# Kernel optimization log

Hardware: AMD Instinct MI355X
Metric: run time of the kernel (lower is better)

Reference implementation:

```python
import jax, jax.numpy as jnp
import numpy as np

B, L = 4, 2048
D_Q = D_K = D_V = 512
D_MODEL = 512
H = 8  # heads; head dim = D_MODEL // H = 64


def _conv1x1(x, W, b):
    # Conv1d with kernel_size=1 == pointwise linear over channels.
    # x: (B, C_in, L), W: (C_out, C_in), b: (C_out,) -> (B, C_out, L)
    return jnp.einsum('oc,bcl->bol', W, x) + b[None, :, None]


def setup_inputs() -> dict:
    key = jax.random.key(0)
    ks = jax.random.split(key, 12)
    s = 0.02
    return {
        'q': jax.random.normal(ks[0], (B, D_Q, L), jnp.float32),
        'k': jax.random.normal(ks[1], (B, D_K, L), jnp.float32),
        'v': jax.random.normal(ks[2], (B, D_V, L), jnp.float32),
        'input_mask': jnp.ones((B, 1, L), jnp.float32),
        'Wq': jax.random.normal(ks[3], (D_MODEL, D_Q), jnp.float32) * s,
        'bq': jax.random.normal(ks[4], (D_MODEL,), jnp.float32) * s,
        'Wk': jax.random.normal(ks[5], (D_MODEL, D_K), jnp.float32) * s,
        'bk': jax.random.normal(ks[6], (D_MODEL,), jnp.float32) * s,
        'Wv': jax.random.normal(ks[7], (D_MODEL, D_V), jnp.float32) * s,
        'bv': jax.random.normal(ks[8], (D_MODEL,), jnp.float32) * s,
        'Wout': jax.random.normal(ks[9], (D_V, D_MODEL), jnp.float32) * s,
        'bout': jax.random.normal(ks[10], (D_V,), jnp.float32) * s,
    }


def reference(q, k, v, input_mask, Wq, bq, Wk, bk, Wv, bv, Wout, bout):
    Bq, _, Lq = q.shape
    qh = _conv1x1(q, Wq, bq).reshape(Bq, H, -1, Lq)  # (B,H,D,L)
    kh = _conv1x1(k, Wk, bk).reshape(Bq, H, -1, Lq)
    vh = _conv1x1(v, Wv, bv).reshape(Bq, H, -1, Lq)
    Dh = qh.shape[2]
    scale = 1.0 / jnp.sqrt(jnp.asarray(Dh, qh.dtype))
    scores = jnp.einsum('bhdl,bhdn->bhln', qh, kh) * scale  # (B,H,L,L)
    # total_mask = ~input_mask[:, 0:1, :].bool(); True -> masked keys
    pad = input_mask[:, 0:1, :] <= 0.5  # (B,1,L_k)
    scores = jnp.where(pad[:, None, :, :], jnp.asarray(-1e9, scores.dtype), scores)
    attn = jax.nn.softmax(scores, axis=-1)  # attn_dropout is None in module
    out = jnp.einsum('bhdn,bhln->bhdl', vh, attn).reshape(Bq, -1, Lq)  # (B,d_model,L)
    # self.dropout is identity at inference; final 1x1 conv projection
    return _conv1x1(out, Wout, bout)  # (B, d_v, L)
```

## Files before the change

kernel.cpp:

```cpp
#include <hip/hip_runtime.h>
#include <hip/hip_bf16.h>


#define BB  4
#define LL  2048
#define CC  512
#define HH  8
#define DHH 64

typedef __attribute__((ext_vector_type(8)))  short bf16x8;
typedef __attribute__((ext_vector_type(4)))  short bf16x4;
typedef __attribute__((ext_vector_type(16))) float f32x16;
typedef __attribute__((ext_vector_type(2)))  unsigned uint2v;
typedef __attribute__((ext_vector_type(4)))  unsigned uint4v;

using us = unsigned short;

#if __has_builtin(__builtin_amdgcn_exp2f)
#define EXP2(x) __builtin_amdgcn_exp2f(x)
#else
#define EXP2(x) __expf(0.6931471805599453f * (x))
#endif

__device__ __forceinline__ us f2bu(float x) {
    unsigned u = __float_as_uint(x);
    return (us)((u + 0x7FFFu + ((u >> 16) & 1u)) >> 16);
}
__device__ __forceinline__ unsigned pk2(float a, float b) {
    unsigned r;
    asm("v_cvt_pk_bf16_f32 %0, %1, %2" : "=v"(r) : "v"(a), "v"(b));
    return r;
}
__device__ __forceinline__ bf16x4 pk4(float a, float b, float c, float d) {
    uint2v u; u[0] = pk2(a, b); u[1] = pk2(c, d);
    return __builtin_bit_cast(bf16x4, u);
}

__device__ __forceinline__ void gl16(const void* g, void* l) {
    __builtin_amdgcn_global_load_lds(
        (const __attribute__((address_space(1))) unsigned int*)g,
        (__attribute__((address_space(3))) unsigned int*)l, 16, 0, 0);
}

__device__ __forceinline__ void transpose_body(const float* __restrict__ X,
                                               us* __restrict__ Xt,
                                               int b, int c0, int n0, int t)
{
    __shared__ float T[64][65];

    const float* Xb = X + ((size_t)b * CC + c0) * LL + n0;
    #pragma unroll
    for (int i = 0; i < 4; ++i) {
        const int cl = (t >> 4) + 16 * i, nl = (t & 15) * 4;
        const float4 f = *(const float4*)(Xb + (size_t)cl * LL + nl);
        T[cl][nl + 0] = f.x; T[cl][nl + 1] = f.y;
        T[cl][nl + 2] = f.z; T[cl][nl + 3] = f.w;
    }
    __syncthreads();
    us* Ot = Xt + ((size_t)b * LL + n0) * CC + c0;
    #pragma unroll
    for (int i = 0; i < 2; ++i) {
        const int nl = (t >> 3) + 32 * i, cb = (t & 7) * 8;
        uint4v u;
        #pragma unroll
        for (int j = 0; j < 4; ++j)
            u[j] = pk2(T[cb + 2 * j][nl], T[cb + 2 * j + 1][nl]);
        *(bf16x8*)(Ot + (size_t)nl * CC + cb) = __builtin_bit_cast(bf16x8, u);
    }
}

__global__ __launch_bounds__(256) void transpose_cvt(const float* __restrict__ X,
                                                     us* __restrict__ Xt)
{
    transpose_body(X, Xt, blockIdx.z, blockIdx.y * 64, blockIdx.x * 64, threadIdx.x);
}

__global__ __launch_bounds__(256) void transpose_cvt3(
    const float* __restrict__ Xq, const float* __restrict__ Xk,
    const float* __restrict__ Xv,
    us* __restrict__ X0, us* __restrict__ X1, us* __restrict__ X2)
{
    const int z = blockIdx.z, which = z >> 2, b = z & 3;
    const float* X = which == 0 ? Xq : (which == 1 ? Xk : Xv);
    us* Xt = which == 0 ? X0 : (which == 1 ? X1 : X2);
    transpose_body(X, Xt, b, blockIdx.y * 64, blockIdx.x * 64, threadIdx.x);
}

__global__ __launch_bounds__(256) void cvt_w4(const float* __restrict__ W0,
                                              const float* __restrict__ W1,
                                              const float* __restrict__ W2,
                                              const float* __restrict__ W3,
                                              us* __restrict__ out)
{
    const float* Ws[4] = {W0, W1, W2, W3};
    const float* W = Ws[blockIdx.y];
    us* O = out + (size_t)blockIdx.y * (CC * CC);
    const int i = (blockIdx.x * 256 + threadIdx.x) * 8;
    const float4 f0 = *(const float4*)(W + i);
    const float4 f1 = *(const float4*)(W + i + 4);
    uint4v u;
    u[0] = pk2(f0.x, f0.y); u[1] = pk2(f0.z, f0.w);
    u[2] = pk2(f1.x, f1.y); u[3] = pk2(f1.z, f1.w);
    *(bf16x8*)(O + i) = __builtin_bit_cast(bf16x8, u);
}

__device__ __forceinline__ void proj_body(const us* __restrict__ Xb,
                                          const us* __restrict__ Wm,
                                          const float* __restrict__ bias,
                                          float scale, void* __restrict__ Yv,
                                          int b, int n0, int m0, int t, int mode)
{
    const int lane = t & 63, wave = t >> 6;
    const int quad2 = lane >> 5, l31 = lane & 31;
    const int wr = (wave >> 1) * 64, wc = (wave & 1) * 64;

    __shared__ __align__(16) char PS[32768];
    __shared__ float biasS[128];

    f32x16 acc[2][2];
    #pragma unroll
    for (int mi = 0; mi < 2; ++mi)
        #pragma unroll
        for (int ni = 0; ni < 2; ++ni)
            #pragma unroll
            for (int e = 0; e < 16; ++e) acc[mi][ni][e] = 0.f;

    if (t < 128) biasS[t] = bias[m0 + t];

    const int rdA = quad2 * 2048 + (wr + l31) * 16;
    const int rdB = 16384 + quad2 * 2048 + (wc + l31) * 16;

    for (int k0 = 0; k0 < CC; k0 += 64) {
        #pragma unroll
        for (int i = 0; i < 4; ++i) {
            const int sg = i * 4 + wave;
            const int r0 = (sg & 1) * 64, bk = sg >> 1;
            gl16(Wm + (size_t)(r0 + lane) * CC + k0 + bk * 8, PS + sg * 1024);
            gl16(Xb + (size_t)(n0 + r0 + lane) * CC + k0 + bk * 8,
                 PS + 16384 + sg * 1024);
        }
        __syncthreads();

        __builtin_amdgcn_s_setprio(1);
        #pragma unroll
        for (int ks = 0; ks < 4; ++ks) {
            const bf16x8 af0 = *(const bf16x8*)(PS + rdA + ks * 4096);
            const bf16x8 af1 = *(const bf16x8*)(PS + rdA + ks * 4096 + 512);
            const bf16x8 bf0 = *(const bf16x8*)(PS + rdB + ks * 4096);
            const bf16x8 bf1 = *(const bf16x8*)(PS + rdB + ks * 4096 + 512);
            acc[0][0] = __builtin_amdgcn_mfma_f32_32x32x16_bf16(af0, bf0, acc[0][0], 0, 0, 0);
            acc[0][1] = __builtin_amdgcn_mfma_f32_32x32x16_bf16(af0, bf1, acc[0][1], 0, 0, 0);
            acc[1][0] = __builtin_amdgcn_mfma_f32_32x32x16_bf16(af1, bf0, acc[1][0], 0, 0, 0);
            acc[1][1] = __builtin_amdgcn_mfma_f32_32x32x16_bf16(af1, bf1, acc[1][1], 0, 0, 0);
        }
        __builtin_amdgcn_s_setprio(0);
        __syncthreads();
    }

    #pragma unroll
    for (int mi = 0; mi < 2; ++mi)
        #pragma unroll
        for (int ni = 0; ni < 2; ++ni) {
            const int nloc = wc + ni * 32 + l31;
            if (mode == 0) {
                us* Y = (us*)Yv;
                #pragma unroll
                for (int rg2 = 0; rg2 < 4; ++rg2) {
                    const int rbase = wr + mi * 32 + 8 * rg2 + 4 * quad2;
                    float v0 = (acc[mi][ni][rg2 * 4 + 0] + biasS[rbase + 0]) * scale;
                    float v1 = (acc[mi][ni][rg2 * 4 + 1] + biasS[rbase + 1]) * scale;
                    float v2 = (acc[mi][ni][rg2 * 4 + 2] + biasS[rbase + 2]) * scale;
                    float v3 = (acc[mi][ni][rg2 * 4 + 3] + biasS[rbase + 3]) * scale;
                    const int mg = m0 + rbase;
                    const int h = mg >> 6, d = mg & 63;
                    *(bf16x4*)(Y + (((size_t)(b * HH + h) * LL) + n0 + nloc) * DHH + d) =
                        pk4(v0, v1, v2, v3);
                }
            } else {
                #pragma unroll
                for (int reg = 0; reg < 16; ++reg) {
                    const int row = (reg & 3) + 8 * (reg >> 2) + 4 * quad2;
                    const int mloc = wr + mi * 32 + row;
                    const float v = (acc[mi][ni][reg] + biasS[mloc]) * scale;
                    const size_t addr = ((size_t)b * CC + m0 + mloc) * LL + n0 + nloc;
                    if (mode == 1) ((us*)Yv)[addr] = f2bu(v);
                    else           ((float*)Yv)[addr] = v;
                }
            }
        }
}

template <int MODE>
__global__ __launch_bounds__(256, 3) void proj_gemm(const us* __restrict__ Xt,
                                                    const us* __restrict__ Wb,
                                                    const float* __restrict__ bias,
                                                    float scale,
                                                    void* __restrict__ Yv)
{
    const int b = blockIdx.z, n0 = blockIdx.x * 128, m0 = blockIdx.y * 128;
    proj_body(Xt + (size_t)b * LL * CC, Wb + (size_t)m0 * CC, bias, scale, Yv,
              b, n0, m0, threadIdx.x, MODE);
}

__global__ __launch_bounds__(256, 3) void proj_gemm3(
    const us* __restrict__ X0, const us* __restrict__ X1, const us* __restrict__ X2,
    const us* __restrict__ Wb4,
    const float* __restrict__ bq, const float* __restrict__ bk,
    const float* __restrict__ bv, float scale_q,
    us* __restrict__ qh, us* __restrict__ kh, us* __restrict__ vh)
{
    const int z = blockIdx.z, which = z >> 2, b = z & 3;
    const int n0 = blockIdx.x * 128, m0 = blockIdx.y * 128;
    const us* Xt = which == 0 ? X0 : (which == 1 ? X1 : X2);
    const us* Wb = Wb4 + (size_t)which * (CC * CC);
    const float* bias = which == 0 ? bq : (which == 1 ? bk : bv);
    const float scale = which == 0 ? scale_q : 1.0f;
    us* Yv = which == 0 ? qh : (which == 1 ? kh : vh);
    const int mode = (which == 2) ? 1 : 0;
    proj_body(Xt + (size_t)b * LL * CC, Wb + (size_t)m0 * CC, bias, scale,
              (void*)Yv, b, n0, m0, threadIdx.x, mode);
}

__global__ __launch_bounds__(512, 4) void attn_fwd(
    const us* __restrict__ Qh,
    const us* __restrict__ Kh,
    const us* __restrict__ Vh,
    const float* __restrict__ mask,
    us* __restrict__ ctx)
{
    const int bh = blockIdx.x;
    const int b = bh >> 3, h = bh & 7;
    const int qb = blockIdx.y;
    const int t = threadIdx.x, lane = t & 63, wave = t >> 6;
    const int half = wave >> 2, wv = wave & 3;
    const int quad2 = lane >> 5, l31 = lane & 31;

    __shared__ __align__(16) char SM[81920];

    const float* mb = mask + (size_t)b * LL;
    const int g0 = half * 16;

    const us* Qg = Qh + ((size_t)bh * LL + qb * 128) * DHH;
    #pragma unroll
    for (int i = 0; i < 2; ++i) {
        const int c = t + i * 512, row = c & 127, bk = c >> 7;
        *(bf16x8*)(SM + c * 16) = *(const bf16x8*)(Qg + row * DHH + bk * 8);
    }

    const us* Kbase = Kh + (size_t)bh * LL * DHH;
    const us* Vbase = Vh + ((size_t)b * CC + h * DHH) * LL;
    char* KH = SM + 16384 + half * 16384;
    char* VH = SM + 49152 + half * 16384;

    {
        const int n1 = g0 * 64;
        #pragma unroll
        for (int i = 0; i < 2; ++i) {
            const int sg = i * 4 + wv;
            gl16(Kbase + (size_t)(n1 + lane) * DHH + sg * 8, KH + sg * 1024);
            gl16(Vbase + (size_t)lane * LL + n1 + sg * 8, VH + sg * 1024);
        }
    }
    float mval = mb[g0 * 64 + lane];
    __syncthreads();

    f32x16 of[2];
    #pragma unroll
    for (int mt = 0; mt < 2; ++mt)
        #pragma unroll
        for (int e = 0; e < 16; ++e) of[mt][e] = 0.f;
    float l_run = 0.f;

    const int rdKV = quad2 * 1024 + l31 * 16;
    const int qrd  = quad2 * 2048 + (wv * 32 + l31) * 16;

    for (int itl = 0; itl < 16; ++itl) {
        const int cur = itl & 1;
        const char* Kc = KH + cur * 8192;
        const char* Vc = VH + cur * 8192;

        float mnext = 0.f;
        if (itl + 1 < 16) {
            const int n1 = (g0 + itl + 1) * 64;
            char* Kn = KH + (1 - cur) * 8192;
            char* Vn = VH + (1 - cur) * 8192;
            #pragma unroll
            for (int i = 0; i < 2; ++i) {
                const int sg = i * 4 + wv;
                gl16(Kbase + (size_t)(n1 + lane) * DHH + sg * 8, Kn + sg * 1024);
                gl16(Vbase + (size_t)lane * LL + n1 + sg * 8, Vn + sg * 1024);
            }
            mnext = mb[(size_t)(g0 + itl + 1) * 64 + lane];
        }

        f32x16 sf[2];
        #pragma unroll
        for (int mt = 0; mt < 2; ++mt)
            #pragma unroll
            for (int e = 0; e < 16; ++e) sf[mt][e] = 0.f;
        __builtin_amdgcn_s_setprio(1);
        #pragma unroll
        for (int ks = 0; ks < 4; ++ks) {
            const bf16x8 qk = *(const bf16x8*)(SM + qrd + ks * 4096);
            #pragma unroll
            for (int mt = 0; mt < 2; ++mt) {
                const bf16x8 af = *(const bf16x8*)(Kc + rdKV + ks * 2048 + mt * 512);
                sf[mt] = __builtin_amdgcn_mfma_f32_32x32x16_bf16(af, qk, sf[mt], 0, 0, 0);
            }
        }
        __builtin_amdgcn_s_setprio(0);

        const unsigned long long mw = __ballot(mval > 0.5f);
        const bool masked = (mw != 0xFFFFFFFFFFFFFFFFull);
        float ps = 0.f;
        #pragma unroll
        for (int j = 0; j < 4; ++j) {
            const int mt = j >> 1, g = j & 1;
            float p[8];
            #pragma unroll
            for (int el = 0; el < 8; ++el) p[el] = EXP2(sf[mt][8 * g + el]);
            if (masked) {
                #pragma unroll
                for (int el = 0; el < 8; ++el) {
                    const int row = 32 * mt + 16 * g + (el & 3) + 8 * (el >> 2) + 4 * quad2;
                    p[el] = ((mw >> row) & 1ull) ? p[el] : 0.f;
                }
            }
            ps += ((p[0] + p[1]) + (p[2] + p[3])) + ((p[4] + p[5]) + (p[6] + p[7]));
            unsigned w0 = pk2(p[0], p[1]);
            unsigned w1 = pk2(p[2], p[3]);
            unsigned w2 = pk2(p[4], p[5]);
            unsigned w3 = pk2(p[6], p[7]);
            asm("v_permlane32_swap_b32 %0, %1" : "+v"(w0), "+v"(w2));
            asm("v_permlane32_swap_b32 %0, %1" : "+v"(w1), "+v"(w3));
            uint4v u; u[0] = w0; u[1] = w1; u[2] = w2; u[3] = w3;
            const bf16x8 pf = __builtin_bit_cast(bf16x8, u);
            __builtin_amdgcn_s_setprio(1);
            of[0] = __builtin_amdgcn_mfma_f32_32x32x16_bf16(
                *(const bf16x8*)(Vc + rdKV + j * 2048), pf, of[0], 0, 0, 0);
            of[1] = __builtin_amdgcn_mfma_f32_32x32x16_bf16(
                *(const bf16x8*)(Vc + rdKV + j * 2048 + 512), pf, of[1], 0, 0, 0);
            __builtin_amdgcn_s_setprio(0);
        }
        ps += __shfl_xor(ps, 32, 64);
        l_run += ps;
        mval = mnext;

        __syncthreads();
    }

    float4* OS = (float4*)SM;
    float*  LS = (float*)(SM + 32768);
    const int qg = qb * 128 + wv * 32;
    if (half == 1) {
        #pragma unroll
        for (int mt = 0; mt < 2; ++mt)
            #pragma unroll
            for (int r4 = 0; r4 < 4; ++r4) {
                float4 v;
                v.x = of[mt][r4 * 4 + 0]; v.y = of[mt][r4 * 4 + 1];
                v.z = of[mt][r4 * 4 + 2]; v.w = of[mt][r4 * 4 + 3];
                OS[(wv * 8 + mt * 4 + r4) * 64 + lane] = v;
            }
        LS[wv * 64 + lane] = l_run;
    }
    __syncthreads();
    if (half == 0) {
        l_run += LS[wv * 64 + lane];
        const float inv = 1.0f / l_run;
        us* Cb = ctx + (size_t)b * LL * CC;
        const int q = qg + l31;
        #pragma unroll
        for (int mt = 0; mt < 2; ++mt)
            #pragma unroll
            for (int r4 = 0; r4 < 4; ++r4) {
                const float4 v = OS[(wv * 8 + mt * 4 + r4) * 64 + lane];
                const int d = 32 * mt + 8 * r4 + 4 * quad2;
                *(bf16x4*)(Cb + (size_t)q * CC + h * DHH + d) =
                    pk4((of[mt][r4 * 4 + 0] + v.x) * inv,
                        (of[mt][r4 * 4 + 1] + v.y) * inv,
                        (of[mt][r4 * 4 + 2] + v.z) * inv,
                        (of[mt][r4 * 4 + 3] + v.w) * inv);
            }
    }
}

extern "C" void kernel_launch(void* const* d_in, const int* in_sizes, int n_in,
                              void* d_out, int out_size, void* d_ws, size_t ws_size,
                              hipStream_t stream)
{
    const float* q    = (const float*)d_in[0];
    const float* k    = (const float*)d_in[1];
    const float* v    = (const float*)d_in[2];
    const float* mask = (const float*)d_in[3];
    const float* Wq   = (const float*)d_in[4];
    const float* bq   = (const float*)d_in[5];
    const float* Wk   = (const float*)d_in[6];
    const float* bk   = (const float*)d_in[7];
    const float* Wv   = (const float*)d_in[8];
    const float* bv   = (const float*)d_in[9];
    const float* Wout = (const float*)d_in[10];
    const float* bout = (const float*)d_in[11];

    const size_t TSZ  = (size_t)BB * CC * LL;
    const size_t WSZ  = (size_t)4 * CC * CC;
    const float SCALE_Q = 0.125f * 1.4426950408889634f;

    const dim3 tb(256), gb(256);

    if (ws_size >= (6 * TSZ + WSZ) * sizeof(us)) {
        us* X0  = (us*)d_ws;
        us* X1  = X0 + TSZ;
        us* X2  = X1 + TSZ;
        us* qh  = X2 + TSZ;
        us* kh  = qh + TSZ;
        us* vh  = kh + TSZ;
        us* Wb  = vh + TSZ;
        us* ctx = X0;

        cvt_w4<<<dim3(CC * CC / 2048, 4), tb, 0, stream>>>(Wq, Wk, Wv, Wout, Wb);
        transpose_cvt3<<<dim3(LL / 64, CC / 64, 12), tb, 0, stream>>>(q, k, v, X0, X1, X2);
        proj_gemm3<<<dim3(LL / 128, CC / 128, 12), gb, 0, stream>>>(
            X0, X1, X2, Wb, bq, bk, bv, SCALE_Q, qh, kh, vh);
        attn_fwd<<<dim3(HH * BB, LL / 128), dim3(512), 0, stream>>>(qh, kh, vh, mask, ctx);
        proj_gemm<2><<<dim3(LL / 128, CC / 128, BB), gb, 0, stream>>>(
            ctx, Wb + 3 * (size_t)CC * CC, bout, 1.0f, d_out);
    } else {
        us* Xt  = (us*)d_ws;
        us* qh  = Xt + TSZ;
        us* kh  = qh + TSZ;
        us* vh  = kh + TSZ;
        us* Wb  = vh + TSZ;
        us* ctx = Xt;

        const dim3 tg(LL / 64, CC / 64, BB), gg(LL / 128, CC / 128, BB);

        cvt_w4<<<dim3(CC * CC / 2048, 4), tb, 0, stream>>>(Wq, Wk, Wv, Wout, Wb);
        transpose_cvt<<<tg, tb, 0, stream>>>(q, Xt);
        proj_gemm<0><<<gg, gb, 0, stream>>>(Xt, Wb + 0 * (size_t)CC * CC, bq, SCALE_Q, (void*)qh);
        transpose_cvt<<<tg, tb, 0, stream>>>(k, Xt);
        proj_gemm<0><<<gg, gb, 0, stream>>>(Xt, Wb + 1 * (size_t)CC * CC, bk, 1.0f, (void*)kh);
        transpose_cvt<<<tg, tb, 0, stream>>>(v, Xt);
        proj_gemm<1><<<gg, gb, 0, stream>>>(Xt, Wb + 2 * (size_t)CC * CC, bv, 1.0f, (void*)vh);
        attn_fwd<<<dim3(HH * BB, LL / 128), dim3(512), 0, stream>>>(qh, kh, vh, mask, ctx);
        proj_gemm<2><<<gg, gb, 0, stream>>>(ctx, Wb + 3 * (size_t)CC * CC, bout, 1.0f, d_out);
    }
}
```

Measured before the change: 218.7 us.

## Register-prefetch double-buffered projection GEMM with swizzled LDS; interleave attention QK and PV

Replaces the projection GEMM's single-buffer global_load_lds staging with register prefetch of the next K tile into a double-buffered, XOR-swizzled LDS layout, dropping one barrier per step. Occupancy hint drops from 3 to 2 blocks per SM to allow the larger LDS footprint and registers. The attention kernel computes scores per 32-row half and feeds each straight into its PV MFMAs, cutting live score registers, and uses incremented pointers instead of recomputed addresses. The trade is fewer resident blocks and more VGPRs for the prefetch buffers.

```diff
diff --git a/kernel.cpp b/kernel.cpp
--- a/kernel.cpp
+++ b/kernel.cpp
@@ -21,6 +21,8 @@
 #else
 #define EXP2(x) __expf(0.6931471805599453f * (x))
 #endif
+
+__device__ __forceinline__ int swz(int r) { return (r + (r >> 3)) & 7; }
 
 __device__ __forceinline__ us f2bu(float x) {
     unsigned u = __float_as_uint(x);
@@ -114,7 +116,8 @@
     const int quad2 = lane >> 5, l31 = lane & 31;
     const int wr = (wave >> 1) * 64, wc = (wave & 1) * 64;
 
-    __shared__ __align__(16) char PS[32768];
+    __shared__ us As[2][128 * 64];
+    __shared__ us Bs[2][128 * 64];
     __shared__ float biasS[128];
 
     f32x16 acc[2][2];
@@ -127,33 +130,54 @@
 
     if (t < 128) biasS[t] = bias[m0 + t];
 
-    const int rdA = quad2 * 2048 + (wr + l31) * 16;
-    const int rdB = 16384 + quad2 * 2048 + (wc + l31) * 16;
-
-    for (int k0 = 0; k0 < CC; k0 += 64) {
-        #pragma unroll
-        for (int i = 0; i < 4; ++i) {
-            const int sg = i * 4 + wave;
-            const int r0 = (sg & 1) * 64, bk = sg >> 1;
-            gl16(Wm + (size_t)(r0 + lane) * CC + k0 + bk * 8, PS + sg * 1024);
-            gl16(Xb + (size_t)(n0 + r0 + lane) * CC + k0 + bk * 8,
-                 PS + 16384 + sg * 1024);
-        }
-        __syncthreads();
+    #pragma unroll
+    for (int i = 0; i < 4; ++i) {
+        const int id = i * 256 + t, r = id >> 3, bk = id & 7;
+        *(bf16x8*)(As[0] + r * 64 + ((bk ^ swz(r)) * 8)) =
+            *(const bf16x8*)(Wm + (size_t)r * CC + bk * 8);
+        *(bf16x8*)(Bs[0] + r * 64 + ((bk ^ swz(r)) * 8)) =
+            *(const bf16x8*)(Xb + (size_t)(n0 + r) * CC + bk * 8);
+    }
+    __syncthreads();
+
+    for (int it = 0; it < CC / 64; ++it) {
+        const int cur = it & 1, k1 = (it + 1) * 64;
+
+        bf16x8 apre[4], bpre[4];
+        if (it + 1 < CC / 64) {
+            #pragma unroll
+            for (int i = 0; i < 4; ++i) {
+                const int id = i * 256 + t, r = id >> 3, bk = id & 7;
+                apre[i] = *(const bf16x8*)(Wm + (size_t)r * CC + k1 + bk * 8);
+                bpre[i] = *(const bf16x8*)(Xb + (size_t)(n0 + r) * CC + k1 + bk * 8);
+            }
+        }
 
         __builtin_amdgcn_s_setprio(1);
         #pragma unroll
         for (int ks = 0; ks < 4; ++ks) {
-            const bf16x8 af0 = *(const bf16x8*)(PS + rdA + ks * 4096);
-            const bf16x8 af1 = *(const bf16x8*)(PS + rdA + ks * 4096 + 512);
-            const bf16x8 bf0 = *(const bf16x8*)(PS + rdB + ks * 4096);
-            const bf16x8 bf1 = *(const bf16x8*)(PS + rdB + ks * 4096 + 512);
+            const int bk = quad2 + 2 * ks;
+            const int ra0 = wr + l31, ra1 = ra0 + 32;
+            const int rb0 = wc + l31, rb1 = rb0 + 32;
+            const bf16x8 af0 = *(const bf16x8*)(As[cur] + ra0 * 64 + ((bk ^ swz(ra0)) * 8));
+            const bf16x8 af1 = *(const bf16x8*)(As[cur] + ra1 * 64 + ((bk ^ swz(ra1)) * 8));
+            const bf16x8 bf0 = *(const bf16x8*)(Bs[cur] + rb0 * 64 + ((bk ^ swz(rb0)) * 8));
+            const bf16x8 bf1 = *(const bf16x8*)(Bs[cur] + rb1 * 64 + ((bk ^ swz(rb1)) * 8));
             acc[0][0] = __builtin_amdgcn_mfma_f32_32x32x16_bf16(af0, bf0, acc[0][0], 0, 0, 0);
             acc[0][1] = __builtin_amdgcn_mfma_f32_32x32x16_bf16(af0, bf1, acc[0][1], 0, 0, 0);
             acc[1][0] = __builtin_amdgcn_mfma_f32_32x32x16_bf16(af1, bf0, acc[1][0], 0, 0, 0);
             acc[1][1] = __builtin_amdgcn_mfma_f32_32x32x16_bf16(af1, bf1, acc[1][1], 0, 0, 0);
         }
         __builtin_amdgcn_s_setprio(0);
+
+        if (it + 1 < CC / 64) {
+            #pragma unroll
+            for (int i = 0; i < 4; ++i) {
+                const int id = i * 256 + t, r = id >> 3, bk = id & 7;
+                *(bf16x8*)(As[1 - cur] + r * 64 + ((bk ^ swz(r)) * 8)) = apre[i];
+                *(bf16x8*)(Bs[1 - cur] + r * 64 + ((bk ^ swz(r)) * 8)) = bpre[i];
+            }
+        }
         __syncthreads();
     }
 
@@ -191,7 +215,7 @@
 }
 
 template <int MODE>
-__global__ __launch_bounds__(256, 3) void proj_gemm(const us* __restrict__ Xt,
+__global__ __launch_bounds__(256, 2) void proj_gemm(const us* __restrict__ Xt,
                                                     const us* __restrict__ Wb,
                                                     const float* __restrict__ bias,
                                                     float scale,
@@ -202,7 +226,7 @@
               b, n0, m0, threadIdx.x, MODE);
 }
 
-__global__ __launch_bounds__(256, 3) void proj_gemm3(
+__global__ __launch_bounds__(256, 2) void proj_gemm3(
     const us* __restrict__ X0, const us* __restrict__ X1, const us* __restrict__ X2,
     const us* __restrict__ Wb4,
     const float* __restrict__ bq, const float* __restrict__ bk,
@@ -247,21 +271,19 @@
         *(bf16x8*)(SM + c * 16) = *(const bf16x8*)(Qg + row * DHH + bk * 8);
     }
 
-    const us* Kbase = Kh + (size_t)bh * LL * DHH;
-    const us* Vbase = Vh + ((size_t)b * CC + h * DHH) * LL;
     char* KH = SM + 16384 + half * 16384;
     char* VH = SM + 49152 + half * 16384;
 
-    {
-        const int n1 = g0 * 64;
-        #pragma unroll
-        for (int i = 0; i < 2; ++i) {
-            const int sg = i * 4 + wv;
-            gl16(Kbase + (size_t)(n1 + lane) * DHH + sg * 8, KH + sg * 1024);
-            gl16(Vbase + (size_t)lane * LL + n1 + sg * 8, VH + sg * 1024);
-        }
-    }
-    float mval = mb[g0 * 64 + lane];
+    const us* kp = Kh + (size_t)bh * LL * DHH + ((size_t)(g0 * 64) + lane) * DHH + wv * 8;
+    const us* vp = Vh + ((size_t)b * CC + h * DHH) * LL + (size_t)lane * LL + g0 * 64 + wv * 8;
+    const float* mp = mb + g0 * 64 + lane;
+
+    gl16(kp,      KH + wv * 1024);
+    gl16(kp + 32, KH + (wv + 4) * 1024);
+    gl16(vp,      VH + wv * 1024);
+    gl16(vp + 32, VH + (wv + 4) * 1024);
+    kp += 64 * DHH; vp += 64;
+    float mval = *mp; mp += 64;
     __syncthreads();
 
     f32x16 of[2];
@@ -281,66 +303,63 @@
 
         float mnext = 0.f;
         if (itl + 1 < 16) {
-            const int n1 = (g0 + itl + 1) * 64;
             char* Kn = KH + (1 - cur) * 8192;
             char* Vn = VH + (1 - cur) * 8192;
-            #pragma unroll
-            for (int i = 0; i < 2; ++i) {
-                const int sg = i * 4 + wv;
-                gl16(Kbase + (size_t)(n1 + lane) * DHH + sg * 8, Kn + sg * 1024);
-                gl16(Vbase + (size_t)lane * LL + n1 + sg * 8, Vn + sg * 1024);
-            }
-            mnext = mb[(size_t)(g0 + itl + 1) * 64 + lane];
-        }
-
-        f32x16 sf[2];
-        #pragma unroll
-        for (int mt = 0; mt < 2; ++mt)
-            #pragma unroll
-            for (int e = 0; e < 16; ++e) sf[mt][e] = 0.f;
-        __builtin_amdgcn_s_setprio(1);
-        #pragma unroll
-        for (int ks = 0; ks < 4; ++ks) {
-            const bf16x8 qk = *(const bf16x8*)(SM + qrd + ks * 4096);
-            #pragma unroll
-            for (int mt = 0; mt < 2; ++mt) {
-                const bf16x8 af = *(const bf16x8*)(Kc + rdKV + ks * 2048 + mt * 512);
-                sf[mt] = __builtin_amdgcn_mfma_f32_32x32x16_bf16(af, qk, sf[mt], 0, 0, 0);
-            }
-        }
-        __builtin_amdgcn_s_setprio(0);
+            gl16(kp,      Kn + wv * 1024);
+            gl16(kp + 32, Kn + (wv + 4) * 1024);
+            gl16(vp,      Vn + wv * 1024);
+            gl16(vp + 32, Vn + (wv + 4) * 1024);
+            kp += 64 * DHH; vp += 64;
+            mnext = *mp; mp += 64;
+        }
 
         const unsigned long long mw = __ballot(mval > 0.5f);
         const bool masked = (mw != 0xFFFFFFFFFFFFFFFFull);
         float ps = 0.f;
-        #pragma unroll
-        for (int j = 0; j < 4; ++j) {
-            const int mt = j >> 1, g = j & 1;
-            float p[8];
-            #pragma unroll
-            for (int el = 0; el < 8; ++el) p[el] = EXP2(sf[mt][8 * g + el]);
-            if (masked) {
+
+        #pragma unroll
+        for (int mt = 0; mt < 2; ++mt) {
+            f32x16 sf;
+            #pragma unroll
+            for (int e = 0; e < 16; ++e) sf[e] = 0.f;
+            __builtin_amdgcn_s_setprio(1);
+            #pragma unroll
+            for (int ks = 0; ks < 4; ++ks) {
+                const bf16x8 qk = *(const bf16x8*)(SM + qrd + ks * 4096);
+                const bf16x8 af = *(const bf16x8*)(Kc + rdKV + ks * 2048 + mt * 512);
+                sf = __builtin_amdgcn_mfma_f32_32x32x16_bf16(af, qk, sf, 0, 0, 0);
+            }
+            __builtin_amdgcn_s_setprio(0);
+
+            #pragma unroll
+            for (int g = 0; g < 2; ++g) {
+                float p[8];
                 #pragma unroll
-                for (int el = 0; el < 8; ++el) {
-                    const int row = 32 * mt + 16 * g + (el & 3) + 8 * (el >> 2) + 4 * quad2;
-                    p[el] = ((mw >> row) & 1ull) ? p[el] : 0.f;
+                for (int el = 0; el < 8; ++el) p[el] = EXP2(sf[8 * g + el]);
+                if (masked) {
+                    #pragma unroll
+                    for (int el = 0; el < 8; ++el) {
+                        const int row = 32 * mt + 16 * g + (el & 3) + 8 * (el >> 2) + 4 * quad2;
+                        p[el] = ((mw >> row) & 1ull) ? p[el] : 0.f;
+                    }
                 }
-            }
-            ps += ((p[0] + p[1]) + (p[2] + p[3])) + ((p[4] + p[5]) + (p[6] + p[7]));
-            unsigned w0 = pk2(p[0], p[1]);
-            unsigned w1 = pk2(p[2], p[3]);
-            unsigned w2 = pk2(p[4], p[5]);
-            unsigned w3 = pk2(p[6], p[7]);
-            asm("v_permlane32_swap_b32 %0, %1" : "+v"(w0), "+v"(w2));
-            asm("v_permlane32_swap_b32 %0, %1" : "+v"(w1), "+v"(w3));
-            uint4v u; u[0] = w0; u[1] = w1; u[2] = w2; u[3] = w3;
-            const bf16x8 pf = __builtin_bit_cast(bf16x8, u);
-            __builtin_amdgcn_s_setprio(1);
-            of[0] = __builtin_amdgcn_mfma_f32_32x32x16_bf16(
-                *(const bf16x8*)(Vc + rdKV + j * 2048), pf, of[0], 0, 0, 0);
-            of[1] = __builtin_amdgcn_mfma_f32_32x32x16_bf16(
-                *(const bf16x8*)(Vc + rdKV + j * 2048 + 512), pf, of[1], 0, 0, 0);
-            __builtin_amdgcn_s_setprio(0);
+                ps += ((p[0] + p[1]) + (p[2] + p[3])) + ((p[4] + p[5]) + (p[6] + p[7]));
+                unsigned w0 = pk2(p[0], p[1]);
+                unsigned w1 = pk2(p[2], p[3]);
+                unsigned w2 = pk2(p[4], p[5]);
+                unsigned w3 = pk2(p[6], p[7]);
+                asm("v_permlane32_swap_b32 %0, %1" : "+v"(w0), "+v"(w2));
+                asm("v_permlane32_swap_b32 %0, %1" : "+v"(w1), "+v"(w3));
+                uint4v u; u[0] = w0; u[1] = w1; u[2] = w2; u[3] = w3;
+                const bf16x8 pf = __builtin_bit_cast(bf16x8, u);
+                const int j = 2 * mt + g;
+                __builtin_amdgcn_s_setprio(1);
+                of[0] = __builtin_amdgcn_mfma_f32_32x32x16_bf16(
+                    *(const bf16x8*)(Vc + rdKV + j * 2048), pf, of[0], 0, 0, 0);
+                of[1] = __builtin_amdgcn_mfma_f32_32x32x16_bf16(
+                    *(const bf16x8*)(Vc + rdKV + j * 2048 + 512), pf, of[1], 0, 0, 0);
+                __builtin_amdgcn_s_setprio(0);
+            }
         }
         ps += __shfl_xor(ps, 32, 64);
         l_run += ps;
```

After: 201.9 us. 1.08x faster.
